# Performance work log

Hardware: AMD Instinct MI355X
Metric: run time of the kernel (lower is better)

The kernel has to match this reference:

```python
import jax, jax.numpy as jnp
import numpy as np

NSITES = 100000
NYEARS = 20
NVIS = 2
HDIM = 64


def setup_inputs() -> dict:
    key = jax.random.key(0)
    ks = jax.random.split(key, 10)
    def w(k, shape, fan_in):
        return (jax.random.normal(k, shape, jnp.float32) / np.sqrt(fan_in)).astype(jnp.float32)
    return {
        "sxy0": jax.random.normal(ks[0], (1, NSITES, 1), jnp.float32),
        "sxy": jax.random.normal(ks[1], (NSITES, NYEARS - 1, 1), jnp.float32),
        "oxy": jax.random.normal(ks[2], (NSITES, NYEARS, NVIS), jnp.float32),
        # to_h0: Linear(1 -> 64)
        "W_h0": w(ks[3], (HDIM, 1), 1), "b_h0": jnp.zeros((HDIM,), jnp.float32),
        # to_h1: Linear(64 -> 64)
        "W_h1": w(ks[4], (HDIM, HDIM), HDIM), "b_h1": jnp.zeros((HDIM,), jnp.float32),
        # to_hrnn: RNN(input=1, hidden=64, relu)
        "W_ih": w(ks[5], (HDIM, 1), 1), "b_ih": jnp.zeros((HDIM,), jnp.float32),
        "W_hh": w(ks[6], (HDIM, HDIM), HDIM), "b_hh": jnp.zeros((HDIM,), jnp.float32),
        # to_psi0 / to_psi: Linear(64 -> 1)
        "W_psi0": w(ks[7], (1, HDIM), HDIM), "b_psi0": jnp.zeros((1,), jnp.float32),
        "W_psi": w(ks[8], (1, HDIM), HDIM), "b_psi": jnp.zeros((1,), jnp.float32),
        # to_p: Linear(65 -> 1)
        "W_p": w(ks[9], (1, HDIM + 1), HDIM + 1), "b_p": jnp.zeros((1,), jnp.float32),
    }


def reference(sxy0, sxy, oxy, W_h0, b_h0, W_h1, b_h1, W_ih, b_ih, W_hh, b_hh,
              W_psi0, b_psi0, W_psi, b_psi, W_p, b_p):
    # site embeddings -> initial hidden state
    hs = jax.nn.elu(sxy0 @ W_h0.T + b_h0)            # [1, N, H]
    h0 = jax.nn.elu(hs @ W_h1.T + b_h1)              # [1, N, H]

    # single-layer relu RNN, batch_first: sxy [N, T, 1], h0 [1, N, H]
    xs = jnp.swapaxes(sxy, 0, 1)                     # [T, N, 1]
    def step(h, x):
        h_new = jax.nn.relu(x @ W_ih.T + b_ih + h @ W_hh.T + b_hh)
        return h_new, h_new
    _, h_seq = jax.lax.scan(step, h0[0], xs)         # [T, N, H]
    h_out = jnp.swapaxes(h_seq, 0, 1)                # [N, T, H]

    psi0_out = jax.nn.sigmoid(h0 @ W_psi0.T + b_psi0)   # [1, N, 1]
    psi_out = jax.nn.sigmoid(h_out @ W_psi.T + b_psi)   # [N, T, 1]

    # detection prob p[i, t, j] = sigmoid(to_p(cat(H[i, t], oxy[i, t, j])))
    # where H[:, 0] = h0 and H[:, t] = h_out[:, t-1] for t >= 1
    H = jnp.concatenate([h0[0][:, None, :], h_out], axis=1)  # [N, Y, H]
    logits = H @ W_p[:, :HDIM].T + oxy * W_p[0, HDIM] + b_p  # [N, Y, NVIS]
    p = jax.nn.sigmoid(logits)
    return psi0_out, psi_out, p
```

## Files before the change

kernel.cpp:

```cpp
#include <hip/hip_runtime.h>
#include <math.h>

#define NSITES 100000
#define NYEARS 20
#define HDIM 64
#define WSTR 72

typedef __bf16 bf16x8 __attribute__((ext_vector_type(8)));
typedef float f32x4 __attribute__((ext_vector_type(4)));

__device__ __forceinline__ float sigmoidf_(float x) { return 1.0f / (1.0f + __expf(-x)); }
__device__ __forceinline__ float eluf_(float x) { return x > 0.0f ? x : __expf(x) - 1.0f; }

__device__ __forceinline__ unsigned pack2_(float a, float b) {
    union { __bf16 h; unsigned short u; } x, y;
    x.h = (__bf16)a; y.h = (__bf16)b;
    return ((unsigned)y.u << 16) | (unsigned)x.u;
}

__device__ __forceinline__ bf16x8 cvt8_(const float* p) {
    float4 a = ((const float4*)p)[0];
    float4 b = ((const float4*)p)[1];
    bf16x8 r;
    r[0] = (__bf16)a.x; r[1] = (__bf16)a.y; r[2] = (__bf16)a.z; r[3] = (__bf16)a.w;
    r[4] = (__bf16)b.x; r[5] = (__bf16)b.y; r[6] = (__bf16)b.z; r[7] = (__bf16)b.w;
    return r;
}

__device__ __forceinline__ bf16x8 ldsfrag_(const unsigned short* b, int row, int off) {
    union { bf16x8 v; uint4 u; } r;
    r.u = *(const uint4*)&b[row * WSTR + off];
    return r.v;
}

__device__ __forceinline__ bf16x8 pack_bf_(f32x4 lo, f32x4 hi) {
    bf16x8 r;
    r[0] = (__bf16)lo[0]; r[1] = (__bf16)lo[1]; r[2] = (__bf16)lo[2]; r[3] = (__bf16)lo[3];
    r[4] = (__bf16)hi[0]; r[5] = (__bf16)hi[1]; r[6] = (__bf16)hi[2]; r[7] = (__bf16)hi[3];
    return r;
}

__global__ __launch_bounds__(256, 2)
void rnet_kernel(const float* __restrict__ sxy0,
                 const float* __restrict__ sxy,
                 const float* __restrict__ oxy,
                 const float* __restrict__ W_h0, const float* __restrict__ b_h0,
                 const float* __restrict__ W_h1, const float* __restrict__ b_h1,
                 const float* __restrict__ W_ih, const float* __restrict__ b_ih,
                 const float* __restrict__ W_hh, const float* __restrict__ b_hh,
                 const float* __restrict__ W_psi0, const float* __restrict__ b_psi0,
                 const float* __restrict__ W_psi, const float* __restrict__ b_psi,
                 const float* __restrict__ W_p, const float* __restrict__ b_p,
                 float* __restrict__ out)
{
    const int tid  = threadIdx.x;
    const int lane = tid & 63;
    const int wv   = tid >> 6;
    const int s = lane & 15;
    const int q = lane >> 4;
    const int sq = s >> 2, sr = s & 3;
    const int base = blockIdx.x * 64;
    const int sl   = wv * 16 + s;
    const int site = base + sl;
    const int site_ld = site < NSITES ? site : NSITES - 1;

    __shared__ __align__(16) unsigned short wbuf[2 * 64 * WSTR];
    __shared__ __align__(16) float xs_sh[64 * 19];
    unsigned short* const whh_l = wbuf;
    unsigned short* const wh1_l = wbuf + 64 * WSTR;
    float* const pL   = (float*)wbuf;
    float* const psiL = (float*)wbuf + 64 * 20;

    float* __restrict__ out_psi0 = out;
    float* __restrict__ out_psi  = out + NSITES;
    float* __restrict__ out_p    = out + 20 * NSITES;

    {
        const float4* whg = (const float4*)W_hh;
        const float4* w1g = (const float4*)W_h1;
#pragma unroll
        for (int j = 0; j < 4; ++j) {
            int e4 = j * 256 + tid;
            int row = e4 >> 4, c4 = e4 & 15;
            float4 a = whg[e4];
            uint2 pa; pa.x = pack2_(a.x, a.y); pa.y = pack2_(a.z, a.w);
            *(uint2*)&whh_l[row * WSTR + c4 * 4] = pa;
            float4 b = w1g[e4];
            uint2 pb; pb.x = pack2_(b.x, b.y); pb.y = pack2_(b.z, b.w);
            *(uint2*)&wh1_l[row * WSTR + c4 * 4] = pb;
        }
#pragma unroll
        for (int r = 0; r < 5; ++r) {
            int i = r * 256 + tid;
            if (i < 64 * 19) {
                int srow = i / 19, c = i - srow * 19;
                int gsite = base + srow; if (gsite >= NSITES) gsite = NSITES - 1;
                xs_sh[i] = sxy[(size_t)gsite * 19 + c];
            }
        }
    }
    __syncthreads();

    bf16x8 bf[2];
    {
        const float s0v = sxy0[site_ld];
        bf16x8 bf0[2];
#pragma unroll
        for (int kt = 0; kt < 2; ++kt) {
            const float* wp = W_h0 + kt * 32 + q * 8;
            const float* bp = b_h0 + kt * 32 + q * 8;
            float4 w0 = ((const float4*)wp)[0], w1 = ((const float4*)wp)[1];
            float4 c0 = ((const float4*)bp)[0], c1 = ((const float4*)bp)[1];
            float v[8];
            v[0] = eluf_(fmaf(s0v, w0.x, c0.x)); v[1] = eluf_(fmaf(s0v, w0.y, c0.y));
            v[2] = eluf_(fmaf(s0v, w0.z, c0.z)); v[3] = eluf_(fmaf(s0v, w0.w, c0.w));
            v[4] = eluf_(fmaf(s0v, w1.x, c1.x)); v[5] = eluf_(fmaf(s0v, w1.y, c1.y));
            v[6] = eluf_(fmaf(s0v, w1.z, c1.z)); v[7] = eluf_(fmaf(s0v, w1.w, c1.w));
#pragma unroll
            for (int j = 0; j < 8; ++j) bf0[kt][j] = (__bf16)v[j];
        }

        f32x4 acc[4];
#pragma unroll
        for (int mt = 0; mt < 4; ++mt) {
            const int dr = 32 * (mt >> 1) + 8 * q + 4 * (mt & 1);
            float4 b1 = *(const float4*)(b_h1 + dr);
            acc[mt][0] = b1.x; acc[mt][1] = b1.y; acc[mt][2] = b1.z; acc[mt][3] = b1.w;
        }
#pragma unroll
        for (int kt = 0; kt < 2; ++kt)
#pragma unroll
            for (int mt = 0; mt < 4; ++mt) {
                const int ar = 32 * (mt >> 1) + 8 * sq + 4 * (mt & 1) + sr;
                bf16x8 a = ldsfrag_(wh1_l, ar, kt * 32 + q * 8);
                acc[mt] = __builtin_amdgcn_mfma_f32_16x16x32_bf16(a, bf0[kt], acc[mt], 0, 0, 0);
            }
        f32x4 e[4];
#pragma unroll
        for (int mt = 0; mt < 4; ++mt)
#pragma unroll
            for (int r = 0; r < 4; ++r) e[mt][r] = eluf_(acc[mt][r]);
        bf[0] = pack_bf_(e[0], e[1]);
        bf[1] = pack_bf_(e[2], e[3]);
    }

    bf16x8 a_hh[4][2];
#pragma unroll
    for (int mt = 0; mt < 4; ++mt) {
        const int ar = 32 * (mt >> 1) + 8 * sq + 4 * (mt & 1) + sr;
#pragma unroll
        for (int kt = 0; kt < 2; ++kt)
            a_hh[mt][kt] = ldsfrag_(whh_l, ar, kt * 32 + q * 8);
    }

    __syncthreads();

    bf16x8 a_head[2];
    {
        const float* hrow = (s == 1) ? W_p : ((s == 2) ? W_psi0 : W_psi);
#pragma unroll
        for (int kt = 0; kt < 2; ++kt) a_head[kt] = cvt8_(hrow + kt * 32 + q * 8);
    }
    f32x4 biasD[4], wihD[4];
#pragma unroll
    for (int mt = 0; mt < 4; ++mt) {
        const int dr = 32 * (mt >> 1) + 8 * q + 4 * (mt & 1);
        float4 bi = *(const float4*)(b_ih + dr);
        float4 bh = *(const float4*)(b_hh + dr);
        float4 wi = *(const float4*)(W_ih + dr);
        biasD[mt][0] = bi.x + bh.x; biasD[mt][1] = bi.y + bh.y;
        biasD[mt][2] = bi.z + bh.z; biasD[mt][3] = bi.w + bh.w;
        wihD[mt][0] = wi.x; wihD[mt][1] = wi.y; wihD[mt][2] = wi.z; wihD[mt][3] = wi.w;
    }
    f32x4 headC;
    headC[0] = (q == 0) ? b_psi[0]  : 0.0f;
    headC[1] = (q == 0) ? b_p[0]    : 0.0f;
    headC[2] = (q == 0) ? b_psi0[0] : 0.0f;
    headC[3] = 0.0f;

    float x = xs_sh[sl * 19];
#pragma unroll 1
    for (int t = 1; t < NYEARS; ++t) {
        float x_next = (t < NYEARS - 1) ? xs_sh[sl * 19 + t] : 0.0f;

        f32x4 acc[4], accH;
#pragma unroll
        for (int mt = 0; mt < 4; ++mt)
            acc[mt] = __builtin_amdgcn_mfma_f32_16x16x32_bf16(a_hh[mt][0], bf[0], biasD[mt], 0, 0, 0);
        accH = __builtin_amdgcn_mfma_f32_16x16x32_bf16(a_head[0], bf[0], headC, 0, 0, 0);
#pragma unroll
        for (int mt = 0; mt < 4; ++mt)
            acc[mt] = __builtin_amdgcn_mfma_f32_16x16x32_bf16(a_hh[mt][1], bf[1], acc[mt], 0, 0, 0);
        accH = __builtin_amdgcn_mfma_f32_16x16x32_bf16(a_head[1], bf[1], accH, 0, 0, 0);

        f32x4 hn[4];
#pragma unroll
        for (int mt = 0; mt < 4; ++mt)
#pragma unroll
            for (int r = 0; r < 4; ++r)
                hn[mt][r] = fmaxf(fmaf(x, wihD[mt][r], acc[mt][r]), 0.0f);
        bf[0] = pack_bf_(hn[0], hn[1]);
        bf[1] = pack_bf_(hn[2], hn[3]);

        if (q == 0) {
            pL[sl * 20 + (t - 1)]   = accH[1];
            psiL[sl * 20 + (t - 1)] = accH[0];
            if (t == 1) psiL[sl * 20] = accH[2];
        }
        x = x_next;
    }

    {
        f32x4 accH = __builtin_amdgcn_mfma_f32_16x16x32_bf16(a_head[0], bf[0], headC, 0, 0, 0);
        accH = __builtin_amdgcn_mfma_f32_16x16x32_bf16(a_head[1], bf[1], accH, 0, 0, 0);
        if (q == 0) {
            pL[sl * 20 + 19]   = accH[1];
            psiL[sl * 20 + 19] = accH[0];
        }
    }

    __syncthreads();

    const float wpo = W_p[HDIM];
    if (tid < 64 && base + tid < NSITES) out_psi0[base + tid] = sigmoidf_(psiL[tid * 20]);
#pragma unroll
    for (int r = 0; r < 5; ++r) {
        int i = r * 256 + tid;
        if (i < 64 * 19 && (size_t)base * 19 + i < (size_t)NSITES * 19) {
            int s2 = i / 19, c = i - s2 * 19;
            out_psi[(size_t)base * 19 + i] = sigmoidf_(psiL[s2 * 20 + c + 1]);
        }
    }
    const float4* oxy_b = (const float4*)(oxy + (size_t)base * 40);
    float4* outp_b = (float4*)(out_p + (size_t)base * 40);
    const int p4max = (NSITES * 40) / 4;
#pragma unroll
    for (int r = 0; r < 3; ++r) {
        int i4 = r * 256 + tid;
        if (i4 < 640 && blockIdx.x * 640 + i4 < p4max) {
            float4 ox = oxy_b[i4];
            float lg0 = pL[i4 * 2];
            float lg1 = pL[i4 * 2 + 1];
            float4 pv;
            pv.x = sigmoidf_(fmaf(wpo, ox.x, lg0));
            pv.y = sigmoidf_(fmaf(wpo, ox.y, lg0));
            pv.z = sigmoidf_(fmaf(wpo, ox.z, lg1));
            pv.w = sigmoidf_(fmaf(wpo, ox.w, lg1));
            outp_b[i4] = pv;
        }
    }
}

extern "C" void kernel_launch(void* const* d_in, const int* in_sizes, int n_in,
                              void* d_out, int out_size, void* d_ws, size_t ws_size,
                              hipStream_t stream) {
    const float* sxy0   = (const float*)d_in[0];
    const float* sxy    = (const float*)d_in[1];
    const float* oxy    = (const float*)d_in[2];
    const float* W_h0   = (const float*)d_in[3];
    const float* b_h0   = (const float*)d_in[4];
    const float* W_h1   = (const float*)d_in[5];
    const float* b_h1   = (const float*)d_in[6];
    const float* W_ih   = (const float*)d_in[7];
    const float* b_ih   = (const float*)d_in[8];
    const float* W_hh   = (const float*)d_in[9];
    const float* b_hh   = (const float*)d_in[10];
    const float* W_psi0 = (const float*)d_in[11];
    const float* b_psi0 = (const float*)d_in[12];
    const float* W_psi  = (const float*)d_in[13];
    const float* b_psi  = (const float*)d_in[14];
    const float* W_p    = (const float*)d_in[15];
    const float* b_p    = (const float*)d_in[16];

    float* out = (float*)d_out;

    dim3 block(256);
    dim3 grid((NSITES + 63) / 64);
    rnet_kernel<<<grid, block, 0, stream>>>(
        sxy0, sxy, oxy, W_h0, b_h0, W_h1, b_h1, W_ih, b_ih, W_hh, b_hh,
        W_psi0, b_psi0, W_psi, b_psi, W_p, b_p, out);
}
```

Baseline: 137.6 us.

## Switch RNN MFMA path to fp16 with packed half2 epilogue and direct sxy loads

Replaces the bf16 MFMA operands with fp16 and does the recurrent epilogue (input term, add and relu) in packed half2 arithmetic, cutting per-step conversion and VALU work on the serial critical path. It also drops the shared-memory staging of sxy and reads each site's inputs straight from global memory inside the loop. This trades bf16 range for fp16 precision in the hidden-state update, and the per-step global loads are uncoalesced and may add latency to the recurrence.

```diff
diff --git a/kernel.cpp b/kernel.cpp
--- a/kernel.cpp
+++ b/kernel.cpp
@@ -6,39 +6,35 @@
 #define HDIM 64
 #define WSTR 72
 
-typedef __bf16 bf16x8 __attribute__((ext_vector_type(8)));
+typedef _Float16 f16x8 __attribute__((ext_vector_type(8)));
+typedef _Float16 hx2   __attribute__((ext_vector_type(2)));
 typedef float f32x4 __attribute__((ext_vector_type(4)));
 
 __device__ __forceinline__ float sigmoidf_(float x) { return 1.0f / (1.0f + __expf(-x)); }
 __device__ __forceinline__ float eluf_(float x) { return x > 0.0f ? x : __expf(x) - 1.0f; }
 
-__device__ __forceinline__ unsigned pack2_(float a, float b) {
-    union { __bf16 h; unsigned short u; } x, y;
-    x.h = (__bf16)a; y.h = (__bf16)b;
+__device__ __forceinline__ unsigned pack2h_(float a, float b) {
+    union { _Float16 h; unsigned short u; } x, y;
+    x.h = (_Float16)a; y.h = (_Float16)b;
     return ((unsigned)y.u << 16) | (unsigned)x.u;
 }
 
-__device__ __forceinline__ bf16x8 cvt8_(const float* p) {
+__device__ __forceinline__ f16x8 cvt8h_(const float* p) {
     float4 a = ((const float4*)p)[0];
     float4 b = ((const float4*)p)[1];
-    bf16x8 r;
-    r[0] = (__bf16)a.x; r[1] = (__bf16)a.y; r[2] = (__bf16)a.z; r[3] = (__bf16)a.w;
-    r[4] = (__bf16)b.x; r[5] = (__bf16)b.y; r[6] = (__bf16)b.z; r[7] = (__bf16)b.w;
+    f16x8 r;
+    r[0] = (_Float16)a.x; r[1] = (_Float16)a.y; r[2] = (_Float16)a.z; r[3] = (_Float16)a.w;
+    r[4] = (_Float16)b.x; r[5] = (_Float16)b.y; r[6] = (_Float16)b.z; r[7] = (_Float16)b.w;
     return r;
 }
 
-__device__ __forceinline__ bf16x8 ldsfrag_(const unsigned short* b, int row, int off) {
-    union { bf16x8 v; uint4 u; } r;
+__device__ __forceinline__ f16x8 ldsfrag_(const unsigned short* b, int row, int off) {
+    union { f16x8 v; uint4 u; } r;
     r.u = *(const uint4*)&b[row * WSTR + off];
     return r.v;
 }
 
-__device__ __forceinline__ bf16x8 pack_bf_(f32x4 lo, f32x4 hi) {
-    bf16x8 r;
-    r[0] = (__bf16)lo[0]; r[1] = (__bf16)lo[1]; r[2] = (__bf16)lo[2]; r[3] = (__bf16)lo[3];
-    r[4] = (__bf16)hi[0]; r[5] = (__bf16)hi[1]; r[6] = (__bf16)hi[2]; r[7] = (__bf16)hi[3];
-    return r;
-}
+union FragU { hx2 h2[4]; f16x8 v; };
 
 __global__ __launch_bounds__(256, 2)
 void rnet_kernel(const float* __restrict__ sxy0,
@@ -65,7 +61,6 @@
     const int site_ld = site < NSITES ? site : NSITES - 1;
 
     __shared__ __align__(16) unsigned short wbuf[2 * 64 * WSTR];
-    __shared__ __align__(16) float xs_sh[64 * 19];
     unsigned short* const whh_l = wbuf;
     unsigned short* const wh1_l = wbuf + 64 * WSTR;
     float* const pL   = (float*)wbuf;
@@ -83,28 +78,19 @@
             int e4 = j * 256 + tid;
             int row = e4 >> 4, c4 = e4 & 15;
             float4 a = whg[e4];
-            uint2 pa; pa.x = pack2_(a.x, a.y); pa.y = pack2_(a.z, a.w);
+            uint2 pa; pa.x = pack2h_(a.x, a.y); pa.y = pack2h_(a.z, a.w);
             *(uint2*)&whh_l[row * WSTR + c4 * 4] = pa;
             float4 b = w1g[e4];
-            uint2 pb; pb.x = pack2_(b.x, b.y); pb.y = pack2_(b.z, b.w);
+            uint2 pb; pb.x = pack2h_(b.x, b.y); pb.y = pack2h_(b.z, b.w);
             *(uint2*)&wh1_l[row * WSTR + c4 * 4] = pb;
         }
-#pragma unroll
-        for (int r = 0; r < 5; ++r) {
-            int i = r * 256 + tid;
-            if (i < 64 * 19) {
-                int srow = i / 19, c = i - srow * 19;
-                int gsite = base + srow; if (gsite >= NSITES) gsite = NSITES - 1;
-                xs_sh[i] = sxy[(size_t)gsite * 19 + c];
-            }
-        }
     }
     __syncthreads();
 
-    bf16x8 bf[2];
+    f16x8 bf[2];
     {
         const float s0v = sxy0[site_ld];
-        bf16x8 bf0[2];
+        f16x8 bf0[2];
 #pragma unroll
         for (int kt = 0; kt < 2; ++kt) {
             const float* wp = W_h0 + kt * 32 + q * 8;
@@ -117,7 +103,7 @@
             v[4] = eluf_(fmaf(s0v, w1.x, c1.x)); v[5] = eluf_(fmaf(s0v, w1.y, c1.y));
             v[6] = eluf_(fmaf(s0v, w1.z, c1.z)); v[7] = eluf_(fmaf(s0v, w1.w, c1.w));
 #pragma unroll
-            for (int j = 0; j < 8; ++j) bf0[kt][j] = (__bf16)v[j];
+            for (int j = 0; j < 8; ++j) bf0[kt][j] = (_Float16)v[j];
         }
 
         f32x4 acc[4];
@@ -132,19 +118,22 @@
 #pragma unroll
             for (int mt = 0; mt < 4; ++mt) {
                 const int ar = 32 * (mt >> 1) + 8 * sq + 4 * (mt & 1) + sr;
-                bf16x8 a = ldsfrag_(wh1_l, ar, kt * 32 + q * 8);
-                acc[mt] = __builtin_amdgcn_mfma_f32_16x16x32_bf16(a, bf0[kt], acc[mt], 0, 0, 0);
+                f16x8 a = ldsfrag_(wh1_l, ar, kt * 32 + q * 8);
+                acc[mt] = __builtin_amdgcn_mfma_f32_16x16x32_f16(a, bf0[kt], acc[mt], 0, 0, 0);
             }
-        f32x4 e[4];
-#pragma unroll
-        for (int mt = 0; mt < 4; ++mt)
-#pragma unroll
-            for (int r = 0; r < 4; ++r) e[mt][r] = eluf_(acc[mt][r]);
-        bf[0] = pack_bf_(e[0], e[1]);
-        bf[1] = pack_bf_(e[2], e[3]);
-    }
-
-    bf16x8 a_hh[4][2];
+        FragU f0, f1;
+#pragma unroll
+        for (int mt = 0; mt < 4; ++mt) {
+            hx2 plo; plo[0] = (_Float16)eluf_(acc[mt][0]); plo[1] = (_Float16)eluf_(acc[mt][1]);
+            hx2 phi; phi[0] = (_Float16)eluf_(acc[mt][2]); phi[1] = (_Float16)eluf_(acc[mt][3]);
+            if (mt < 2) { f0.h2[mt * 2] = plo; f0.h2[mt * 2 + 1] = phi; }
+            else        { f1.h2[(mt - 2) * 2] = plo; f1.h2[(mt - 2) * 2 + 1] = phi; }
+        }
+        bf[0] = f0.v;
+        bf[1] = f1.v;
+    }
+
+    f16x8 a_hh[4][2];
 #pragma unroll
     for (int mt = 0; mt < 4; ++mt) {
         const int ar = 32 * (mt >> 1) + 8 * sq + 4 * (mt & 1) + sr;
@@ -155,13 +144,14 @@
 
     __syncthreads();
 
-    bf16x8 a_head[2];
+    f16x8 a_head[2];
     {
         const float* hrow = (s == 1) ? W_p : ((s == 2) ? W_psi0 : W_psi);
 #pragma unroll
-        for (int kt = 0; kt < 2; ++kt) a_head[kt] = cvt8_(hrow + kt * 32 + q * 8);
-    }
-    f32x4 biasD[4], wihD[4];
+        for (int kt = 0; kt < 2; ++kt) a_head[kt] = cvt8h_(hrow + kt * 32 + q * 8);
+    }
+    f32x4 biasD[4];
+    hx2 wih2[4][2];
 #pragma unroll
     for (int mt = 0; mt < 4; ++mt) {
         const int dr = 32 * (mt >> 1) + 8 * q + 4 * (mt & 1);
@@ -170,37 +160,46 @@
         float4 wi = *(const float4*)(W_ih + dr);
         biasD[mt][0] = bi.x + bh.x; biasD[mt][1] = bi.y + bh.y;
         biasD[mt][2] = bi.z + bh.z; biasD[mt][3] = bi.w + bh.w;
-        wihD[mt][0] = wi.x; wihD[mt][1] = wi.y; wihD[mt][2] = wi.z; wihD[mt][3] = wi.w;
+        wih2[mt][0][0] = (_Float16)wi.x; wih2[mt][0][1] = (_Float16)wi.y;
+        wih2[mt][1][0] = (_Float16)wi.z; wih2[mt][1][1] = (_Float16)wi.w;
     }
     f32x4 headC;
     headC[0] = (q == 0) ? b_psi[0]  : 0.0f;
     headC[1] = (q == 0) ? b_p[0]    : 0.0f;
     headC[2] = (q == 0) ? b_psi0[0] : 0.0f;
     headC[3] = 0.0f;
-
-    float x = xs_sh[sl * 19];
+    const hx2 z2 = (hx2)(_Float16)0.0f;
+    const float* __restrict__ xs_g = sxy + (size_t)site_ld * 19;
+
+    float x = xs_g[0];
 #pragma unroll 1
     for (int t = 1; t < NYEARS; ++t) {
-        float x_next = (t < NYEARS - 1) ? xs_sh[sl * 19 + t] : 0.0f;
+        float x_next = (t < NYEARS - 1) ? xs_g[t] : 0.0f;
 
         f32x4 acc[4], accH;
 #pragma unroll
         for (int mt = 0; mt < 4; ++mt)
-            acc[mt] = __builtin_amdgcn_mfma_f32_16x16x32_bf16(a_hh[mt][0], bf[0], biasD[mt], 0, 0, 0);
-        accH = __builtin_amdgcn_mfma_f32_16x16x32_bf16(a_head[0], bf[0], headC, 0, 0, 0);
+            acc[mt] = __builtin_amdgcn_mfma_f32_16x16x32_f16(a_hh[mt][0], bf[0], biasD[mt], 0, 0, 0);
+        accH = __builtin_amdgcn_mfma_f32_16x16x32_f16(a_head[0], bf[0], headC, 0, 0, 0);
 #pragma unroll
         for (int mt = 0; mt < 4; ++mt)
-            acc[mt] = __builtin_amdgcn_mfma_f32_16x16x32_bf16(a_hh[mt][1], bf[1], acc[mt], 0, 0, 0);
-        accH = __builtin_amdgcn_mfma_f32_16x16x32_bf16(a_head[1], bf[1], accH, 0, 0, 0);
-
-        f32x4 hn[4];
-#pragma unroll
-        for (int mt = 0; mt < 4; ++mt)
-#pragma unroll
-            for (int r = 0; r < 4; ++r)
-                hn[mt][r] = fmaxf(fmaf(x, wihD[mt][r], acc[mt][r]), 0.0f);
-        bf[0] = pack_bf_(hn[0], hn[1]);
-        bf[1] = pack_bf_(hn[2], hn[3]);
+            acc[mt] = __builtin_amdgcn_mfma_f32_16x16x32_f16(a_hh[mt][1], bf[1], acc[mt], 0, 0, 0);
+        accH = __builtin_amdgcn_mfma_f32_16x16x32_f16(a_head[1], bf[1], accH, 0, 0, 0);
+
+        _Float16 xh = (_Float16)x;
+        hx2 x2; x2[0] = xh; x2[1] = xh;
+        FragU f0, f1;
+#pragma unroll
+        for (int mt = 0; mt < 4; ++mt) {
+            hx2 plo; plo[0] = (_Float16)acc[mt][0]; plo[1] = (_Float16)acc[mt][1];
+            hx2 phi; phi[0] = (_Float16)acc[mt][2]; phi[1] = (_Float16)acc[mt][3];
+            plo = __builtin_elementwise_max(plo + x2 * wih2[mt][0], z2);
+            phi = __builtin_elementwise_max(phi + x2 * wih2[mt][1], z2);
+            if (mt < 2) { f0.h2[mt * 2] = plo; f0.h2[mt * 2 + 1] = phi; }
+            else        { f1.h2[(mt - 2) * 2] = plo; f1.h2[(mt - 2) * 2 + 1] = phi; }
+        }
+        bf[0] = f0.v;
+        bf[1] = f1.v;
 
         if (q == 0) {
             pL[sl * 20 + (t - 1)]   = accH[1];
@@ -211,8 +210,8 @@
     }
 
     {
-        f32x4 accH = __builtin_amdgcn_mfma_f32_16x16x32_bf16(a_head[0], bf[0], headC, 0, 0, 0);
-        accH = __builtin_amdgcn_mfma_f32_16x16x32_bf16(a_head[1], bf[1], accH, 0, 0, 0);
+        f32x4 accH = __builtin_amdgcn_mfma_f32_16x16x32_f16(a_head[0], bf[0], headC, 0, 0, 0);
+        accH = __builtin_amdgcn_mfma_f32_16x16x32_f16(a_head[1], bf[1], accH, 0, 0, 0);
         if (q == 0) {
             pL[sl * 20 + 19]   = accH[1];
             psiL[sl * 20 + 19] = accH[0];
```

Measured after the change: 136.0 us. No clear change (-1.2%).
